# Kernel optimization log

Measured on AMD Instinct MI355X. Metric: run time of the kernel, lower is better.

## Reference

```python
import jax, jax.numpy as jnp
import numpy as np

N_NODES = 100000
N_EDGES = 1600000
N_GRAPHS = 2000
IN_DIM, HID, OUT_DIM, N_CLS = 6, 256, 128, 60
EPS = 1e-5


def setup_inputs() -> dict:
    key = jax.random.key(0)
    ks = jax.random.split(key, 16)
    def lin(k, i, o):
        s = 1.0 / np.sqrt(i)
        k1, k2 = jax.random.split(k)
        return (jax.random.uniform(k1, (i, o), jnp.float32, -s, s),
                jax.random.uniform(k2, (o,), jnp.float32, -s, s))
    W_emb, b_emb = lin(ks[0], IN_DIM, HID)
    Wc1, bc1 = lin(ks[1], HID, HID)
    W2, b2 = lin(ks[2], HID, HID)
    Wc2, bc2 = lin(ks[3], HID, HID)
    W3, b3 = lin(ks[4], HID, OUT_DIM)
    Wcls, bcls = lin(ks[5], OUT_DIM, N_CLS)
    return {
        'node_features': jax.random.normal(ks[6], (N_NODES, IN_DIM), jnp.float32),
        'src': jax.random.randint(ks[7], (N_EDGES,), 0, N_NODES, jnp.int32),
        'dst': jax.random.randint(ks[8], (N_EDGES,), 0, N_NODES, jnp.int32),
        'graph_ids': jnp.sort(jax.random.randint(ks[9], (N_NODES,), 0, N_GRAPHS, jnp.int32)),
        'W_emb': W_emb, 'b_emb': b_emb,
        'Wc1': Wc1, 'bc1': bc1,
        'g1': jnp.ones((HID,), jnp.float32), 'be1': jnp.zeros((HID,), jnp.float32),
        'W2': W2, 'b2': b2,
        'Wc2': Wc2, 'bc2': bc2,
        'g2': jnp.ones((HID,), jnp.float32), 'be2': jnp.zeros((HID,), jnp.float32),
        'W3': W3, 'b3': b3,
        'Wcls': Wcls, 'bcls': bcls,
    }


def _graph_conv(x, W, b, src, dst, dout_isqrt, din_isqrt):
    # DGL GraphConv, norm='both': msg = x_src * dout^-1/2, sum to dst, * din^-1/2, then W, b
    m = x[src] * dout_isqrt[src][:, None]            # [E, H]
    agg = jax.ops.segment_sum(m, dst, num_segments=N_NODES)
    agg = agg * din_isqrt[:, None]
    return agg @ W + b


def _bn(h, g, b):
    # BatchNorm1d, training mode: batch stats over node dim, biased variance
    mu = jnp.mean(h, axis=0)
    var = jnp.mean(jnp.square(h - mu), axis=0)
    return (h - mu) * jax.lax.rsqrt(var + EPS) * g + b


def reference(node_features, src, dst, graph_ids, W_emb, b_emb, Wc1, bc1, g1, be1,
              W2, b2, Wc2, bc2, g2, be2, W3, b3, Wcls, bcls):
    ones_e = jnp.ones((N_EDGES,), jnp.float32)
    dout = jax.ops.segment_sum(ones_e, src, num_segments=N_NODES)
    din = jax.ops.segment_sum(ones_e, dst, num_segments=N_NODES)
    dout_isqrt = jnp.where(dout > 0, jax.lax.rsqrt(jnp.maximum(dout, 1.0)), 0.0)
    din_isqrt = jnp.where(din > 0, jax.lax.rsqrt(jnp.maximum(din, 1.0)), 0.0)

    x = node_features @ W_emb + b_emb                              # [N, H]
    h = x + _graph_conv(x, Wc1, bc1, src, dst, dout_isqrt, din_isqrt)
    h = jax.nn.relu(_bn(h, g1, be1))
    h = h @ W2 + b2
    h = x + _graph_conv(h, Wc2, bc2, src, dst, dout_isqrt, din_isqrt)
    h = jax.nn.relu(_bn(h, g2, be2))
    h = h @ W3 + b3                                                # [N, OUT_DIM]

    # dgl.mean_nodes: per-graph mean of h
    sums = jax.ops.segment_sum(h, graph_ids, num_segments=N_GRAPHS)
    cnts = jax.ops.segment_sum(jnp.ones((N_NODES,), jnp.float32), graph_ids, num_segments=N_GRAPHS)
    y = sums / jnp.maximum(cnts, 1.0)[:, None]                     # [G, OUT_DIM]
    label = y @ Wcls + bcls                                        # [G, N_CLS]
    return h, label
```

## Files before the change

### kernel.cpp

```cpp
#include <hip/hip_runtime.h>

#define NNODES 100000
#define MPAD   100032
#define NEDGES 1600000
#define NGRAPHS 2000
#define HID 256
#define OUTD 128
#define NCLS 60
#define BN_EPS 1e-5f
#define NROWBLK 1563
#define NSCANBLK 98
#define REDBLK 32

typedef __attribute__((ext_vector_type(8))) short bf16x8;
typedef __attribute__((ext_vector_type(4))) float f32x4;

__device__ __forceinline__ float b2f(unsigned short b) {
    unsigned int u = ((unsigned int)b) << 16;
    return __builtin_bit_cast(float, u);
}
__device__ __forceinline__ unsigned short f2b(float f) {
    unsigned int u = __builtin_bit_cast(unsigned int, f);
    u = (u + 0x7FFFu + ((u >> 16) & 1u)) >> 16;
    return (unsigned short)u;
}

__global__ void k_zero_int(int* __restrict__ p, int n) {
    int i = blockIdx.x * blockDim.x + threadIdx.x;
    if (i < n) p[i] = 0;
}

__global__ void k_deg2(const int* __restrict__ src, const int* __restrict__ dst,
                       int* __restrict__ dout, int* __restrict__ din,
                       int* __restrict__ lpos) {
    int e = blockIdx.x * blockDim.x + threadIdx.x;
    if (e < NEDGES) {
        atomicAdd(&dout[src[e]], 1);
        lpos[e] = atomicAdd(&din[dst[e]], 1);
    }
}

__global__ void k_isqrt(const int* __restrict__ dout, const int* __restrict__ din,
                        float* __restrict__ dos, float* __restrict__ dis) {
    int i = blockIdx.x * blockDim.x + threadIdx.x;
    if (i < NNODES) {
        int a = dout[i], b = din[i];
        dos[i] = a > 0 ? 1.0f / sqrtf((float)a) : 0.0f;
        dis[i] = b > 0 ? 1.0f / sqrtf((float)b) : 0.0f;
    }
}

__global__ void k_blk_sum(const int* __restrict__ deg, int* __restrict__ bsum) {
    __shared__ int red[256];
    int blk = blockIdx.x, tid = threadIdx.x;
    int base = blk * 1024;
    int s = 0;
#pragma unroll
    for (int j = 0; j < 4; ++j) {
        int i = base + tid + j * 256;
        if (i < NNODES) s += deg[i];
    }
    red[tid] = s;
    __syncthreads();
    for (int off = 128; off > 0; off >>= 1) {
        if (tid < off) red[tid] += red[tid + off];
        __syncthreads();
    }
    if (tid == 0) bsum[blk] = red[0];
}

__global__ void k_scan_bsum(int* __restrict__ bsum) {
    if (threadIdx.x == 0) {
        int acc = 0;
        for (int i = 0; i < NSCANBLK; ++i) { int v = bsum[i]; bsum[i] = acc; acc += v; }
    }
}

__global__ void k_scan_local(const int* __restrict__ deg, const int* __restrict__ bsum,
                             int* __restrict__ row_ptr) {
    __shared__ int buf[1024];
    int blk = blockIdx.x, tid = threadIdx.x;
    int i = blk * 1024 + tid;
    int v = (i < NNODES) ? deg[i] : 0;
    buf[tid] = v;
    __syncthreads();
    for (int off = 1; off < 1024; off <<= 1) {
        int t = (tid >= off) ? buf[tid - off] : 0;
        __syncthreads();
        buf[tid] += t;
        __syncthreads();
    }
    int inc = buf[tid] + bsum[blk];
    if (i < NNODES) row_ptr[i + 1] = inc;
    if (i == 0) row_ptr[0] = 0;
}

__global__ void k_place(const int* __restrict__ src, const int* __restrict__ dst,
                        const int* __restrict__ lpos, const int* __restrict__ row_ptr,
                        const float* __restrict__ dos, int2* __restrict__ csr_ew) {
    int e = blockIdx.x * blockDim.x + threadIdx.x;
    if (e < NEDGES) {
        int s = src[e];
        csr_ew[row_ptr[dst[e]] + lpos[e]] = make_int2(s, __float_as_int(dos[s]));
    }
}

__global__ void k_wconv(const float* __restrict__ W, unsigned short* __restrict__ Wt,
                        int K, int N) {
    int idx = blockIdx.x * 256 + threadIdx.x;
    if (idx >= N * K) return;
    int n = idx / K, k = idx - n * K;
    Wt[idx] = f2b(W[(size_t)k * N + n]);
}

__global__ void k_small_mm(const float* __restrict__ Wemb, const float* __restrict__ bemb,
                           const float* __restrict__ Wc1, float* __restrict__ M1,
                           float* __restrict__ v1) {
    int c = threadIdx.x;
    int bi = blockIdx.x;
    float acc = 0.f;
    if (bi < 6) {
        for (int k = 0; k < HID; ++k) acc = fmaf(Wemb[bi * HID + k], Wc1[k * HID + c], acc);
        M1[bi * HID + c] = acc;
    } else {
        for (int k = 0; k < HID; ++k) acc = fmaf(bemb[k], Wc1[k * HID + c], acc);
        v1[c] = acc;
    }
}

__global__ void k_agg6(const int* __restrict__ row_ptr, const int2* __restrict__ csr_ew,
                       const float* __restrict__ nf,
                       float* __restrict__ t6, float* __restrict__ u1) {
    int n = blockIdx.x * blockDim.x + threadIdx.x;
    if (n >= NNODES) return;
    float a0 = 0, a1 = 0, a2 = 0, a3 = 0, a4 = 0, a5 = 0, au = 0;
    int s = row_ptr[n], e = row_ptr[n + 1];
    int i = s;
    for (; i + 2 <= e; i += 2) {
        int2 g0 = csr_ew[i], g1 = csr_ew[i + 1];
        float w0 = __int_as_float(g0.y), w1 = __int_as_float(g1.y);
        const float* p0 = nf + (size_t)g0.x * 6;
        const float* p1 = nf + (size_t)g1.x * 6;
        a0 = fmaf(w0, p0[0], a0); a1 = fmaf(w0, p0[1], a1); a2 = fmaf(w0, p0[2], a2);
        a3 = fmaf(w0, p0[3], a3); a4 = fmaf(w0, p0[4], a4); a5 = fmaf(w0, p0[5], a5);
        au += w0;
        a0 = fmaf(w1, p1[0], a0); a1 = fmaf(w1, p1[1], a1); a2 = fmaf(w1, p1[2], a2);
        a3 = fmaf(w1, p1[3], a3); a4 = fmaf(w1, p1[4], a4); a5 = fmaf(w1, p1[5], a5);
        au += w1;
    }
    for (; i < e; ++i) {
        int2 g0 = csr_ew[i];
        float w = __int_as_float(g0.y);
        const float* p = nf + (size_t)g0.x * 6;
        a0 = fmaf(w, p[0], a0); a1 = fmaf(w, p[1], a1); a2 = fmaf(w, p[2], a2);
        a3 = fmaf(w, p[3], a3); a4 = fmaf(w, p[4], a4); a5 = fmaf(w, p[5], a5);
        au += w;
    }
    float* t = t6 + (size_t)n * 6;
    t[0] = a0; t[1] = a1; t[2] = a2; t[3] = a3; t[4] = a4; t[5] = a5;
    u1[n] = au;
}

__global__ __launch_bounds__(256) void k_layer1(
    const float* __restrict__ nf, const float* __restrict__ Wemb, const float* __restrict__ bemb,
    const float* __restrict__ M1, const float* __restrict__ v1, const float* __restrict__ bc1,
    const float* __restrict__ t6, const float* __restrict__ u1, const float* __restrict__ dis,
    unsigned short* __restrict__ H, float* __restrict__ psum, float* __restrict__ psq) {
    __shared__ float s_nf[64][6];
    __shared__ float s_t6[64][6];
    __shared__ float s_u[64];
    __shared__ float s_r[64];
    int blk = blockIdx.x;
    int n0 = blk * 64;
    int tid = threadIdx.x;
    for (int t = tid; t < 384; t += 256) {
        int nl = t / 6, i = t % 6;
        int n = n0 + nl;
        s_nf[nl][i] = (n < NNODES) ? nf[(size_t)n * 6 + i] : 0.f;
        s_t6[nl][i] = (n < NNODES) ? t6[(size_t)n * 6 + i] : 0.f;
    }
    if (tid < 64) {
        int n = n0 + tid;
        s_u[tid] = (n < NNODES) ? u1[n] : 0.f;
        s_r[tid] = (n < NNODES) ? dis[n] : 0.f;
    }
    int c = tid;
    float wc[6], mc[6];
#pragma unroll
    for (int i = 0; i < 6; ++i) { wc[i] = Wemb[i * HID + c]; mc[i] = M1[i * HID + c]; }
    float v1c = v1[c];
    float bsum = bemb[c] + bc1[c];
    __syncthreads();
    float ps = 0.f, pq = 0.f;
    int nmax = min(64, NNODES - n0);
    for (int nl = 0; nl < nmax; ++nl) {
        float nfd = 0.f, td = 0.f;
#pragma unroll
        for (int i = 0; i < 6; ++i) {
            nfd = fmaf(s_nf[nl][i], wc[i], nfd);
            td = fmaf(s_t6[nl][i], mc[i], td);
        }
        float val = nfd + s_r[nl] * (td + s_u[nl] * v1c) + bsum;
        H[(size_t)(n0 + nl) * HID + c] = f2b(val);
        ps += val;
        pq = fmaf(val, val, pq);
    }
    for (int nl = nmax; nl < 64; ++nl) H[(size_t)(n0 + nl) * HID + c] = 0;
    psum[blk * HID + c] = ps;
    psq[blk * HID + c] = pq;
}

__global__ void k_bn_part(const float* __restrict__ psum, const float* __restrict__ psq,
                          double* __restrict__ tmp) {
    int c = threadIdx.x;
    int s = blockIdx.x;
    double a = 0.0, b = 0.0;
    for (int bb = s; bb < NROWBLK; bb += REDBLK) {
        a += psum[bb * HID + c];
        b += psq[bb * HID + c];
    }
    tmp[s * HID + c] = a;
    tmp[(REDBLK + s) * HID + c] = b;
}

__global__ void k_bn_final(const double* __restrict__ tmp, const float* __restrict__ g,
                           const float* __restrict__ be, float* __restrict__ scale,
                           float* __restrict__ shift) {
    int c = threadIdx.x;
    double s = 0.0, q = 0.0;
    for (int i = 0; i < REDBLK; ++i) { s += tmp[i * HID + c]; q += tmp[(REDBLK + i) * HID + c]; }
    double mu = s / (double)NNODES;
    double var = q / (double)NNODES - mu * mu;
    if (var < 0.0) var = 0.0;
    double inv = 1.0 / sqrt(var + (double)BN_EPS);
    float sc = (float)((double)g[c] * inv);
    scale[c] = sc;
    shift[c] = be[c] - (float)mu * sc;
}

template <int NC, bool ATRANS, bool XEPI, bool PART, bool OUTF32>
__global__ __launch_bounds__(256, 2) void k_mgemm(
    const unsigned short* __restrict__ A, const unsigned short* __restrict__ Bt,
    const float* __restrict__ bias,
    const float* __restrict__ scale, const float* __restrict__ shift,
    const float* __restrict__ nf, const float* __restrict__ Wemb, const float* __restrict__ bemb,
    unsigned short* __restrict__ Cb, float* __restrict__ Cf,
    float* __restrict__ psum, float* __restrict__ psq) {
    __shared__ unsigned short As[64 * 256];
    __shared__ unsigned short Bs[64 * 256];
    __shared__ float sSc[HID];
    __shared__ float sSh[HID];
    __shared__ float sNf[64][6];
    __shared__ float sXW[6][HID];
    __shared__ float redS[2][64];
    __shared__ float redQ[2][64];

    int tid = threadIdx.x;
    int rb = blockIdx.x;
    int row0 = rb * 64;

    if (ATRANS) { sSc[tid] = scale[tid]; sSh[tid] = shift[tid]; }
    if (XEPI) {
        for (int t = tid; t < 6 * NC; t += 256) {
            int i = t / NC, cl = t % NC;
            sXW[i][cl] = Wemb[i * HID + cl];
        }
        if (tid < 64) {
            int n = row0 + tid;
#pragma unroll
            for (int i = 0; i < 6; ++i) sNf[tid][i] = (n < NNODES) ? nf[(size_t)n * 6 + i] : 0.f;
        }
    }
    if (ATRANS) __syncthreads();

#pragma unroll
    for (int i = 0; i < 8; ++i) {
        int g = i * 256 + tid;
        int row = g >> 5, kc = g & 31;
        uint4 v = *(const uint4*)(A + (size_t)(row0 + row) * 256 + kc * 8);
        if (ATRANS) {
            unsigned int w[4] = {v.x, v.y, v.z, v.w};
#pragma unroll
            for (int q = 0; q < 4; ++q) {
                int k0 = kc * 8 + q * 2;
                float f0 = b2f((unsigned short)(w[q] & 0xffffu));
                float f1 = b2f((unsigned short)(w[q] >> 16));
                f0 = fmaxf(fmaf(f0, sSc[k0], sSh[k0]), 0.f);
                f1 = fmaxf(fmaf(f1, sSc[k0 + 1], sSh[k0 + 1]), 0.f);
                w[q] = (unsigned int)f2b(f0) | ((unsigned int)f2b(f1) << 16);
            }
            v.x = w[0]; v.y = w[1]; v.z = w[2]; v.w = w[3];
        }
        int pkc = kc ^ (row & 7);
        *(uint4*)(&As[row * 256 + pkc * 8]) = v;
    }

    int w = tid >> 6, lane = tid & 63;
    int wm = w >> 1, wn = w & 1;
    int lrow = lane & 15, lk = lane >> 4;

    for (int cb = 0; cb < NC / 64; ++cb) {
        int c0 = cb * 64;
        if (cb) __syncthreads();
#pragma unroll
        for (int i = 0; i < 8; ++i) {
            int g = i * 256 + tid;
            int row = g >> 5, kc = g & 31;
            uint4 v = *(const uint4*)(Bt + (size_t)(c0 + row) * 256 + kc * 8);
            int pkc = kc ^ (row & 7);
            *(uint4*)(&Bs[row * 256 + pkc * 8]) = v;
        }
        __syncthreads();

        f32x4 acc[2][2] = {};
#pragma unroll
        for (int ks = 0; ks < 8; ++ks) {
            bf16x8 af[2], bfr[2];
#pragma unroll
            for (int fm = 0; fm < 2; ++fm) {
                int r = wm * 32 + fm * 16 + lrow;
                int kc = ks * 4 + lk;
                af[fm] = *(const bf16x8*)(&As[r * 256 + (kc ^ (r & 7)) * 8]);
            }
#pragma unroll
            for (int fn = 0; fn < 2; ++fn) {
                int r = wn * 32 + fn * 16 + lrow;
                int kc = ks * 4 + lk;
                bfr[fn] = *(const bf16x8*)(&Bs[r * 256 + (kc ^ (r & 7)) * 8]);
            }
#pragma unroll
            for (int fm = 0; fm < 2; ++fm)
#pragma unroll
                for (int fn = 0; fn < 2; ++fn)
                    acc[fm][fn] = __builtin_amdgcn_mfma_f32_16x16x32_bf16(af[fm], bfr[fn], acc[fm][fn], 0, 0, 0);
        }

        float pS[2] = {0.f, 0.f}, pQ[2] = {0.f, 0.f};
#pragma unroll
        for (int fn = 0; fn < 2; ++fn) {
            int cl = wn * 32 + fn * 16 + lrow;
            int gc = c0 + cl;
            float bv = bias[gc];
            if (XEPI) bv += bemb[gc];
#pragma unroll
            for (int fm = 0; fm < 2; ++fm) {
#pragma unroll
                for (int r = 0; r < 4; ++r) {
                    int rl = wm * 32 + fm * 16 + lk * 4 + r;
                    int gr = row0 + rl;
                    float val = acc[fm][fn][r] + bv;
                    if (XEPI) {
#pragma unroll
                        for (int l = 0; l < 6; ++l) val = fmaf(sNf[rl][l], sXW[l][gc], val);
                    }
                    if (gr < NNODES) {
                        if (OUTF32) Cf[(size_t)gr * NC + gc] = val;
                        else        Cb[(size_t)gr * NC + gc] = f2b(val);
                        if (PART) { pS[fn] += val; pQ[fn] = fmaf(val, val, pQ[fn]); }
                    }
                }
            }
        }
        if (PART) {
#pragma unroll
            for (int fn = 0; fn < 2; ++fn) {
                float s = pS[fn], q = pQ[fn];
                s += __shfl_xor(s, 16); s += __shfl_xor(s, 32);
                q += __shfl_xor(q, 16); q += __shfl_xor(q, 32);
                if (lk == 0) {
                    int cl = wn * 32 + fn * 16 + lrow;
                    redS[wm][cl] = s;
                    redQ[wm][cl] = q;
                }
            }
            __syncthreads();
            if (tid < 64) {
                psum[(size_t)rb * HID + c0 + tid] = redS[0][tid] + redS[1][tid];
                psq [(size_t)rb * HID + c0 + tid] = redQ[0][tid] + redQ[1][tid];
            }
        }
    }
}

#define ACC8(vv, ww) { \
    a[0] = fmaf(ww, b2f((unsigned short)(vv.x & 0xffffu)), a[0]); \
    a[1] = fmaf(ww, b2f((unsigned short)(vv.x >> 16)),     a[1]); \
    a[2] = fmaf(ww, b2f((unsigned short)(vv.y & 0xffffu)), a[2]); \
    a[3] = fmaf(ww, b2f((unsigned short)(vv.y >> 16)),     a[3]); \
    a[4] = fmaf(ww, b2f((unsigned short)(vv.z & 0xffffu)), a[4]); \
    a[5] = fmaf(ww, b2f((unsigned short)(vv.z >> 16)),     a[5]); \
    a[6] = fmaf(ww, b2f((unsigned short)(vv.w & 0xffffu)), a[6]); \
    a[7] = fmaf(ww, b2f((unsigned short)(vv.w >> 16)),     a[7]); }

__global__ __launch_bounds__(256) void k_agg(const int* __restrict__ row_ptr,
                                             const int2* __restrict__ csr_ew,
                                             const unsigned short* __restrict__ X,
                                             const float* __restrict__ dis,
                                             unsigned short* __restrict__ out) {
    int wid = threadIdx.x >> 6, lane = threadIdx.x & 63;
    int half = lane >> 5, l32 = lane & 31;
    int n = blockIdx.x * 4 + wid;
    if (n >= NNODES) return;
    int s = row_ptr[n], e = row_ptr[n + 1];
    float a[8] = {0.f, 0.f, 0.f, 0.f, 0.f, 0.f, 0.f, 0.f};
    int i = s;
    for (; i + 8 <= e; i += 8) {
        int2 e0 = csr_ew[i + half];
        int2 e1 = csr_ew[i + 2 + half];
        int2 e2 = csr_ew[i + 4 + half];
        int2 e3 = csr_ew[i + 6 + half];
        uint4 v0 = ((const uint4*)(X + (size_t)e0.x * HID))[l32];
        uint4 v1 = ((const uint4*)(X + (size_t)e1.x * HID))[l32];
        uint4 v2 = ((const uint4*)(X + (size_t)e2.x * HID))[l32];
        uint4 v3 = ((const uint4*)(X + (size_t)e3.x * HID))[l32];
        float w0 = __int_as_float(e0.y), w1 = __int_as_float(e1.y);
        float w2 = __int_as_float(e2.y), w3 = __int_as_float(e3.y);
        ACC8(v0, w0) ACC8(v1, w1) ACC8(v2, w2) ACC8(v3, w3)
    }
    for (; i + 2 <= e; i += 2) {
        int2 e0 = csr_ew[i + half];
        uint4 v0 = ((const uint4*)(X + (size_t)e0.x * HID))[l32];
        float w0 = __int_as_float(e0.y);
        ACC8(v0, w0)
    }
    if (i < e && half == 0) {
        int2 e0 = csr_ew[i];
        uint4 v0 = ((const uint4*)(X + (size_t)e0.x * HID))[l32];
        float w0 = __int_as_float(e0.y);
        ACC8(v0, w0)
    }
#pragma unroll
    for (int j = 0; j < 8; ++j) a[j] += __shfl_xor(a[j], 32);
    if (half == 0) {
        float r = dis[n];
        uint4 o;
        o.x = (unsigned)f2b(a[0] * r) | ((unsigned)f2b(a[1] * r) << 16);
        o.y = (unsigned)f2b(a[2] * r) | ((unsigned)f2b(a[3] * r) << 16);
        o.z = (unsigned)f2b(a[4] * r) | ((unsigned)f2b(a[5] * r) << 16);
        o.w = (unsigned)f2b(a[6] * r) | ((unsigned)f2b(a[7] * r) << 16);
        ((uint4*)(out + (size_t)n * HID))[l32] = o;
    }
}

__global__ __launch_bounds__(128) void k_mean_label(const float* __restrict__ Hout,
                                                    const int* __restrict__ gids,
                                                    const float* __restrict__ Wcls,
                                                    const float* __restrict__ bcls,
                                                    float* __restrict__ lab) {
    int g = blockIdx.x;
    int c = threadIdx.x;
    int lo = 0, hi = NNODES;
    while (lo < hi) { int mid = (lo + hi) >> 1; if (gids[mid] < g) lo = mid + 1; else hi = mid; }
    int s = lo;
    hi = NNODES;
    while (lo < hi) { int mid = (lo + hi) >> 1; if (gids[mid] < g + 1) lo = mid + 1; else hi = mid; }
    int e = lo;
    float acc = 0.f;
    for (int n = s; n < e; ++n) acc += Hout[(size_t)n * OUTD + c];
    int cnt = e - s;
    float y = acc / (float)max(cnt, 1);
    __shared__ float ys[OUTD];
    ys[c] = y;
    __syncthreads();
    if (c < NCLS) {
        float a = bcls[c];
        for (int k = 0; k < OUTD; ++k) a = fmaf(ys[k], Wcls[k * NCLS + c], a);
        lab[(size_t)g * NCLS + c] = a;
    }
}

extern "C" void kernel_launch(void* const* d_in, const int* in_sizes, int n_in,
                              void* d_out, int out_size, void* d_ws, size_t ws_size,
                              hipStream_t stream) {
    const float* nf   = (const float*)d_in[0];
    const int*   src  = (const int*)d_in[1];
    const int*   dst  = (const int*)d_in[2];
    const int*   gids = (const int*)d_in[3];
    const float* Wemb = (const float*)d_in[4];
    const float* bemb = (const float*)d_in[5];
    const float* Wc1  = (const float*)d_in[6];
    const float* bc1  = (const float*)d_in[7];
    const float* g1   = (const float*)d_in[8];
    const float* be1  = (const float*)d_in[9];
    const float* W2   = (const float*)d_in[10];
    const float* b2   = (const float*)d_in[11];
    const float* Wc2  = (const float*)d_in[12];
    const float* bc2  = (const float*)d_in[13];
    const float* g2   = (const float*)d_in[14];
    const float* be2  = (const float*)d_in[15];
    const float* W3   = (const float*)d_in[16];
    const float* b3   = (const float*)d_in[17];
    const float* Wcls = (const float*)d_in[18];
    const float* bcls = (const float*)d_in[19];

    float* out_h   = (float*)d_out;
    float* out_lab = out_h + (size_t)NNODES * OUTD;

    float* ws = (float*)d_ws;
    size_t off = 0;
    auto take = [&](size_t n) { float* p = ws + off; off += (n + 63) & ~(size_t)63; return p; };
    unsigned short* actA = (unsigned short*)take((size_t)MPAD * HID / 2);
    unsigned short* actB = (unsigned short*)take((size_t)MPAD * HID / 2);
    unsigned short* Wt2  = (unsigned short*)take(HID * HID / 2);
    unsigned short* Wtc2 = (unsigned short*)take(HID * HID / 2);
    unsigned short* Wt3  = (unsigned short*)take(OUTD * HID / 2);
    int*   deg_out = (int*)take(NNODES);
    int*   deg_in  = (int*)take(NNODES);
    float* dout_is = take(NNODES);
    float* din_is  = take(NNODES);
    int*   row_ptr = (int*)take(NNODES + 1);
    int*   lpos    = (int*)take(NEDGES);
    int2*  csr_ew  = (int2*)take((size_t)NEDGES * 2);
    float* t6      = take((size_t)NNODES * 6);
    float* u1      = take(NNODES);
    float* M1      = take(6 * HID);
    float* v1      = take(HID);
    float* psum    = take((size_t)NROWBLK * HID);
    float* psq     = take((size_t)NROWBLK * HID);
    float* scale1  = take(HID);
    float* shift1  = take(HID);
    float* scale2  = take(HID);
    float* shift2  = take(HID);
    int*   bsum    = (int*)take(128);
    double* bn_tmp = (double*)take(2 * 2 * REDBLK * HID);

    k_zero_int<<<(2 * 100032 + 255) / 256, 256, 0, stream>>>(deg_out, 2 * 100032);
    k_deg2<<<(NEDGES + 255) / 256, 256, 0, stream>>>(src, dst, deg_out, deg_in, lpos);
    k_isqrt<<<(NNODES + 255) / 256, 256, 0, stream>>>(deg_out, deg_in, dout_is, din_is);
    k_blk_sum<<<NSCANBLK, 256, 0, stream>>>(deg_in, bsum);
    k_scan_bsum<<<1, 64, 0, stream>>>(bsum);
    k_scan_local<<<NSCANBLK, 1024, 0, stream>>>(deg_in, bsum, row_ptr);
    k_place<<<(NEDGES + 255) / 256, 256, 0, stream>>>(src, dst, lpos, row_ptr, dout_is, csr_ew);
    k_wconv<<<(HID * HID + 255) / 256, 256, 0, stream>>>(W2, Wt2, HID, HID);
    k_wconv<<<(HID * HID + 255) / 256, 256, 0, stream>>>(Wc2, Wtc2, HID, HID);
    k_wconv<<<(HID * OUTD + 255) / 256, 256, 0, stream>>>(W3, Wt3, HID, OUTD);
    k_small_mm<<<7, 256, 0, stream>>>(Wemb, bemb, Wc1, M1, v1);
    k_agg6<<<(NNODES + 255) / 256, 256, 0, stream>>>(row_ptr, csr_ew, nf, t6, u1);
    k_layer1<<<NROWBLK, 256, 0, stream>>>(nf, Wemb, bemb, M1, v1, bc1, t6, u1, din_is,
                                          actA, psum, psq);
    k_bn_part<<<REDBLK, 256, 0, stream>>>(psum, psq, bn_tmp);
    k_bn_final<<<1, 256, 0, stream>>>(bn_tmp, g1, be1, scale1, shift1);
    k_mgemm<HID, true, false, false, false><<<NROWBLK, 256, 0, stream>>>(
        actA, Wt2, b2, scale1, shift1, nullptr, nullptr, nullptr, actB, nullptr, nullptr, nullptr);
    k_agg<<<NNODES / 4, 256, 0, stream>>>(row_ptr, csr_ew, actB, din_is, actA);
    k_mgemm<HID, false, true, true, false><<<NROWBLK, 256, 0, stream>>>(
        actA, Wtc2, bc2, nullptr, nullptr, nf, Wemb, bemb, actB, nullptr, psum, psq);
    k_bn_part<<<REDBLK, 256, 0, stream>>>(psum, psq, bn_tmp);
    k_bn_final<<<1, 256, 0, stream>>>(bn_tmp, g2, be2, scale2, shift2);
    k_mgemm<OUTD, true, false, false, true><<<NROWBLK, 256, 0, stream>>>(
        actB, Wt3, b3, scale2, shift2, nullptr, nullptr, nullptr, nullptr, out_h, nullptr, nullptr);
    k_mean_label<<<NGRAPHS, OUTD, 0, stream>>>(out_h, gids, Wcls, bcls, out_lab);
}
```

Before: 724.0 us.

## Pre-scale sources by out-degree norm to shrink CSR to bare indices

Moves the per-edge out-degree normalization into the producers: the layer-1 GEMM epilogue scales its rows by dout^-1/2, and the raw features are pre-scaled into a padded 8-float array that also carries the weight for the u-term. The CSR then stores only source indices (4 bytes per edge instead of 8), and both aggregation kernels use plain adds with vectorized float4 loads. It also fuses the isqrt kernel into the block-sum kernel and merges three weight-conversion launches into one. The cost is an extra nf7 pass and an additional bf16 rounding of the pre-scaled activations.

```diff
diff --git a/kernel.cpp b/kernel.cpp
--- a/kernel.cpp
+++ b/kernel.cpp
@@ -40,17 +40,9 @@
     }
 }
 
-__global__ void k_isqrt(const int* __restrict__ dout, const int* __restrict__ din,
-                        float* __restrict__ dos, float* __restrict__ dis) {
-    int i = blockIdx.x * blockDim.x + threadIdx.x;
-    if (i < NNODES) {
-        int a = dout[i], b = din[i];
-        dos[i] = a > 0 ? 1.0f / sqrtf((float)a) : 0.0f;
-        dis[i] = b > 0 ? 1.0f / sqrtf((float)b) : 0.0f;
-    }
-}
-
-__global__ void k_blk_sum(const int* __restrict__ deg, int* __restrict__ bsum) {
+__global__ void k_blk_sum(const int* __restrict__ din, const int* __restrict__ dout,
+                          int* __restrict__ bsum, float* __restrict__ dos,
+                          float* __restrict__ dis) {
     __shared__ int red[256];
     int blk = blockIdx.x, tid = threadIdx.x;
     int base = blk * 1024;
@@ -58,7 +50,13 @@
 #pragma unroll
     for (int j = 0; j < 4; ++j) {
         int i = base + tid + j * 256;
-        if (i < NNODES) s += deg[i];
+        if (i < NNODES) {
+            int b = din[i];
+            int a = dout[i];
+            s += b;
+            dos[i] = a > 0 ? 1.0f / sqrtf((float)a) : 0.0f;
+            dis[i] = b > 0 ? 1.0f / sqrtf((float)b) : 0.0f;
+        }
     }
     red[tid] = s;
     __syncthreads();
@@ -97,20 +95,39 @@
 
 __global__ void k_place(const int* __restrict__ src, const int* __restrict__ dst,
                         const int* __restrict__ lpos, const int* __restrict__ row_ptr,
-                        const float* __restrict__ dos, int2* __restrict__ csr_ew) {
+                        int* __restrict__ csr_e) {
     int e = blockIdx.x * blockDim.x + threadIdx.x;
-    if (e < NEDGES) {
-        int s = src[e];
-        csr_ew[row_ptr[dst[e]] + lpos[e]] = make_int2(s, __float_as_int(dos[s]));
-    }
-}
-
-__global__ void k_wconv(const float* __restrict__ W, unsigned short* __restrict__ Wt,
-                        int K, int N) {
+    if (e < NEDGES) csr_e[row_ptr[dst[e]] + lpos[e]] = src[e];
+}
+
+__global__ void k_nf7(const float* __restrict__ nf, const float* __restrict__ dos,
+                      float* __restrict__ nf7) {
+    int n = blockIdx.x * blockDim.x + threadIdx.x;
+    if (n >= NNODES) return;
+    float w = dos[n];
+    const float* p = nf + (size_t)n * 6;
+    float4 lo = {p[0] * w, p[1] * w, p[2] * w, p[3] * w};
+    float4 hi = {p[4] * w, p[5] * w, w, 0.f};
+    float4* o = (float4*)(nf7 + (size_t)n * 8);
+    o[0] = lo; o[1] = hi;
+}
+
+__global__ void k_wconv3(const float* __restrict__ W2, const float* __restrict__ Wc2,
+                         const float* __restrict__ W3, unsigned short* __restrict__ Wt2,
+                         unsigned short* __restrict__ Wtc2, unsigned short* __restrict__ Wt3) {
     int idx = blockIdx.x * 256 + threadIdx.x;
-    if (idx >= N * K) return;
-    int n = idx / K, k = idx - n * K;
-    Wt[idx] = f2b(W[(size_t)k * N + n]);
+    if (idx < 65536) {
+        int n = idx >> 8, k = idx & 255;
+        Wt2[idx] = f2b(W2[k * 256 + n]);
+    } else if (idx < 131072) {
+        int j = idx - 65536;
+        int n = j >> 8, k = j & 255;
+        Wtc2[j] = f2b(Wc2[k * 256 + n]);
+    } else if (idx < 163840) {
+        int j = idx - 131072;
+        int n = j >> 8, k = j & 255;
+        Wt3[j] = f2b(W3[k * 128 + n]);
+    }
 }
 
 __global__ void k_small_mm(const float* __restrict__ Wemb, const float* __restrict__ bemb,
@@ -128,47 +145,37 @@
     }
 }
 
-__global__ void k_agg6(const int* __restrict__ row_ptr, const int2* __restrict__ csr_ew,
-                       const float* __restrict__ nf,
-                       float* __restrict__ t6, float* __restrict__ u1) {
+__global__ void k_agg6(const int* __restrict__ row_ptr, const int* __restrict__ csr_e,
+                       const float* __restrict__ nf7, float* __restrict__ t7) {
     int n = blockIdx.x * blockDim.x + threadIdx.x;
     if (n >= NNODES) return;
-    float a0 = 0, a1 = 0, a2 = 0, a3 = 0, a4 = 0, a5 = 0, au = 0;
+    float a0 = 0, a1 = 0, a2 = 0, a3 = 0, a4 = 0, a5 = 0, a6 = 0;
     int s = row_ptr[n], e = row_ptr[n + 1];
     int i = s;
     for (; i + 2 <= e; i += 2) {
-        int2 g0 = csr_ew[i], g1 = csr_ew[i + 1];
-        float w0 = __int_as_float(g0.y), w1 = __int_as_float(g1.y);
-        const float* p0 = nf + (size_t)g0.x * 6;
-        const float* p1 = nf + (size_t)g1.x * 6;
-        a0 = fmaf(w0, p0[0], a0); a1 = fmaf(w0, p0[1], a1); a2 = fmaf(w0, p0[2], a2);
-        a3 = fmaf(w0, p0[3], a3); a4 = fmaf(w0, p0[4], a4); a5 = fmaf(w0, p0[5], a5);
-        au += w0;
-        a0 = fmaf(w1, p1[0], a0); a1 = fmaf(w1, p1[1], a1); a2 = fmaf(w1, p1[2], a2);
-        a3 = fmaf(w1, p1[3], a3); a4 = fmaf(w1, p1[4], a4); a5 = fmaf(w1, p1[5], a5);
-        au += w1;
-    }
-    for (; i < e; ++i) {
-        int2 g0 = csr_ew[i];
-        float w = __int_as_float(g0.y);
-        const float* p = nf + (size_t)g0.x * 6;
-        a0 = fmaf(w, p[0], a0); a1 = fmaf(w, p[1], a1); a2 = fmaf(w, p[2], a2);
-        a3 = fmaf(w, p[3], a3); a4 = fmaf(w, p[4], a4); a5 = fmaf(w, p[5], a5);
-        au += w;
-    }
-    float* t = t6 + (size_t)n * 6;
-    t[0] = a0; t[1] = a1; t[2] = a2; t[3] = a3; t[4] = a4; t[5] = a5;
-    u1[n] = au;
+        const float4* p0 = (const float4*)(nf7 + (size_t)csr_e[i] * 8);
+        const float4* p1 = (const float4*)(nf7 + (size_t)csr_e[i + 1] * 8);
+        float4 l0 = p0[0], h0 = p0[1], l1 = p1[0], h1 = p1[1];
+        a0 += l0.x; a1 += l0.y; a2 += l0.z; a3 += l0.w; a4 += h0.x; a5 += h0.y; a6 += h0.z;
+        a0 += l1.x; a1 += l1.y; a2 += l1.z; a3 += l1.w; a4 += h1.x; a5 += h1.y; a6 += h1.z;
+    }
+    if (i < e) {
+        const float4* p0 = (const float4*)(nf7 + (size_t)csr_e[i] * 8);
+        float4 l0 = p0[0], h0 = p0[1];
+        a0 += l0.x; a1 += l0.y; a2 += l0.z; a3 += l0.w; a4 += h0.x; a5 += h0.y; a6 += h0.z;
+    }
+    float4* o = (float4*)(t7 + (size_t)n * 8);
+    o[0] = make_float4(a0, a1, a2, a3);
+    o[1] = make_float4(a4, a5, a6, 0.f);
 }
 
 __global__ __launch_bounds__(256) void k_layer1(
     const float* __restrict__ nf, const float* __restrict__ Wemb, const float* __restrict__ bemb,
     const float* __restrict__ M1, const float* __restrict__ v1, const float* __restrict__ bc1,
-    const float* __restrict__ t6, const float* __restrict__ u1, const float* __restrict__ dis,
+    const float* __restrict__ t7, const float* __restrict__ dis,
     unsigned short* __restrict__ H, float* __restrict__ psum, float* __restrict__ psq) {
     __shared__ float s_nf[64][6];
-    __shared__ float s_t6[64][6];
-    __shared__ float s_u[64];
+    __shared__ float s_t7[64][8];
     __shared__ float s_r[64];
     int blk = blockIdx.x;
     int n0 = blk * 64;
@@ -177,11 +184,11 @@
         int nl = t / 6, i = t % 6;
         int n = n0 + nl;
         s_nf[nl][i] = (n < NNODES) ? nf[(size_t)n * 6 + i] : 0.f;
-        s_t6[nl][i] = (n < NNODES) ? t6[(size_t)n * 6 + i] : 0.f;
-    }
+    }
+    if (tid < 128)
+        ((float4*)s_t7)[tid] = ((const float4*)(t7 + (size_t)n0 * 8))[tid];
     if (tid < 64) {
         int n = n0 + tid;
-        s_u[tid] = (n < NNODES) ? u1[n] : 0.f;
         s_r[tid] = (n < NNODES) ? dis[n] : 0.f;
     }
     int c = tid;
@@ -198,9 +205,9 @@
 #pragma unroll
         for (int i = 0; i < 6; ++i) {
             nfd = fmaf(s_nf[nl][i], wc[i], nfd);
-            td = fmaf(s_t6[nl][i], mc[i], td);
-        }
-        float val = nfd + s_r[nl] * (td + s_u[nl] * v1c) + bsum;
+            td = fmaf(s_t7[nl][i], mc[i], td);
+        }
+        float val = nfd + s_r[nl] * (td + s_t7[nl][6] * v1c) + bsum;
         H[(size_t)(n0 + nl) * HID + c] = f2b(val);
         ps += val;
         pq = fmaf(val, val, pq);
@@ -238,12 +245,13 @@
     shift[c] = be[c] - (float)mu * sc;
 }
 
-template <int NC, bool ATRANS, bool XEPI, bool PART, bool OUTF32>
+template <int NC, bool ATRANS, bool XEPI, bool PART, bool OUTF32, bool RS>
 __global__ __launch_bounds__(256, 2) void k_mgemm(
     const unsigned short* __restrict__ A, const unsigned short* __restrict__ Bt,
     const float* __restrict__ bias,
     const float* __restrict__ scale, const float* __restrict__ shift,
     const float* __restrict__ nf, const float* __restrict__ Wemb, const float* __restrict__ bemb,
+    const float* __restrict__ rs,
     unsigned short* __restrict__ Cb, float* __restrict__ Cf,
     float* __restrict__ psum, float* __restrict__ psq) {
     __shared__ unsigned short As[64 * 256];
@@ -252,6 +260,7 @@
     __shared__ float sSh[HID];
     __shared__ float sNf[64][6];
     __shared__ float sXW[6][HID];
+    __shared__ float sRs[64];
     __shared__ float redS[2][64];
     __shared__ float redQ[2][64];
 
@@ -260,6 +269,10 @@
     int row0 = rb * 64;
 
     if (ATRANS) { sSc[tid] = scale[tid]; sSh[tid] = shift[tid]; }
+    if (RS && tid < 64) {
+        int n = row0 + tid;
+        sRs[tid] = (n < NNODES) ? rs[n] : 0.f;
+    }
     if (XEPI) {
         for (int t = tid; t < 6 * NC; t += 256) {
             int i = t / NC, cl = t % NC;
@@ -353,6 +366,7 @@
 #pragma unroll
                         for (int l = 0; l < 6; ++l) val = fmaf(sNf[rl][l], sXW[l][gc], val);
                     }
+                    if (RS) val *= sRs[rl];
                     if (gr < NNODES) {
                         if (OUTF32) Cf[(size_t)gr * NC + gc] = val;
                         else        Cb[(size_t)gr * NC + gc] = f2b(val);
@@ -382,18 +396,18 @@
     }
 }
 
-#define ACC8(vv, ww) { \
-    a[0] = fmaf(ww, b2f((unsigned short)(vv.x & 0xffffu)), a[0]); \
-    a[1] = fmaf(ww, b2f((unsigned short)(vv.x >> 16)),     a[1]); \
-    a[2] = fmaf(ww, b2f((unsigned short)(vv.y & 0xffffu)), a[2]); \
-    a[3] = fmaf(ww, b2f((unsigned short)(vv.y >> 16)),     a[3]); \
-    a[4] = fmaf(ww, b2f((unsigned short)(vv.z & 0xffffu)), a[4]); \
-    a[5] = fmaf(ww, b2f((unsigned short)(vv.z >> 16)),     a[5]); \
-    a[6] = fmaf(ww, b2f((unsigned short)(vv.w & 0xffffu)), a[6]); \
-    a[7] = fmaf(ww, b2f((unsigned short)(vv.w >> 16)),     a[7]); }
+#define ADD8(vv) { \
+    a[0] += b2f((unsigned short)(vv.x & 0xffffu)); \
+    a[1] += b2f((unsigned short)(vv.x >> 16)); \
+    a[2] += b2f((unsigned short)(vv.y & 0xffffu)); \
+    a[3] += b2f((unsigned short)(vv.y >> 16)); \
+    a[4] += b2f((unsigned short)(vv.z & 0xffffu)); \
+    a[5] += b2f((unsigned short)(vv.z >> 16)); \
+    a[6] += b2f((unsigned short)(vv.w & 0xffffu)); \
+    a[7] += b2f((unsigned short)(vv.w >> 16)); }
 
 __global__ __launch_bounds__(256) void k_agg(const int* __restrict__ row_ptr,
-                                             const int2* __restrict__ csr_ew,
+                                             const int* __restrict__ csr_e,
                                              const unsigned short* __restrict__ X,
                                              const float* __restrict__ dis,
                                              unsigned short* __restrict__ out) {
@@ -405,29 +419,25 @@
     float a[8] = {0.f, 0.f, 0.f, 0.f, 0.f, 0.f, 0.f, 0.f};
     int i = s;
     for (; i + 8 <= e; i += 8) {
-        int2 e0 = csr_ew[i + half];
-        int2 e1 = csr_ew[i + 2 + half];
-        int2 e2 = csr_ew[i + 4 + half];
-        int2 e3 = csr_ew[i + 6 + half];
-        uint4 v0 = ((const uint4*)(X + (size_t)e0.x * HID))[l32];
-        uint4 v1 = ((const uint4*)(X + (size_t)e1.x * HID))[l32];
-        uint4 v2 = ((const uint4*)(X + (size_t)e2.x * HID))[l32];
-        uint4 v3 = ((const uint4*)(X + (size_t)e3.x * HID))[l32];
-        float w0 = __int_as_float(e0.y), w1 = __int_as_float(e1.y);
-        float w2 = __int_as_float(e2.y), w3 = __int_as_float(e3.y);
-        ACC8(v0, w0) ACC8(v1, w1) ACC8(v2, w2) ACC8(v3, w3)
+        int s0 = csr_e[i + half];
+        int s1 = csr_e[i + 2 + half];
+        int s2 = csr_e[i + 4 + half];
+        int s3 = csr_e[i + 6 + half];
+        uint4 v0 = ((const uint4*)(X + (size_t)s0 * HID))[l32];
+        uint4 v1 = ((const uint4*)(X + (size_t)s1 * HID))[l32];
+        uint4 v2 = ((const uint4*)(X + (size_t)s2 * HID))[l32];
+        uint4 v3 = ((const uint4*)(X + (size_t)s3 * HID))[l32];
+        ADD8(v0) ADD8(v1) ADD8(v2) ADD8(v3)
     }
     for (; i + 2 <= e; i += 2) {
-        int2 e0 = csr_ew[i + half];
-        uint4 v0 = ((const uint4*)(X + (size_t)e0.x * HID))[l32];
-        float w0 = __int_as_float(e0.y);
-        ACC8(v0, w0)
+        int s0 = csr_e[i + half];
+        uint4 v0 = ((const uint4*)(X + (size_t)s0 * HID))[l32];
+        ADD8(v0)
     }
     if (i < e && half == 0) {
-        int2 e0 = csr_ew[i];
-        uint4 v0 = ((const uint4*)(X + (size_t)e0.x * HID))[l32];
-        float w0 = __int_as_float(e0.y);
-        ACC8(v0, w0)
+        int s0 = csr_e[i];
+        uint4 v0 = ((const uint4*)(X + (size_t)s0 * HID))[l32];
+        ADD8(v0)
     }
 #pragma unroll
     for (int j = 0; j < 8; ++j) a[j] += __shfl_xor(a[j], 32);
@@ -510,9 +520,9 @@
     float* din_is  = take(NNODES);
     int*   row_ptr = (int*)take(NNODES + 1);
     int*   lpos    = (int*)take(NEDGES);
-    int2*  csr_ew  = (int2*)take((size_t)NEDGES * 2);
-    float* t6      = take((size_t)NNODES * 6);
-    float* u1      = take(NNODES);
+    int*   csr_e   = (int*)take(NEDGES);
+    float* nf7     = take((size_t)NNODES * 8);
+    float* t7      = take((size_t)MPAD * 8);
     float* M1      = take(6 * HID);
     float* v1      = take(HID);
     float* psum    = take((size_t)NROWBLK * HID);
@@ -526,28 +536,29 @@
 
     k_zero_int<<<(2 * 100032 + 255) / 256, 256, 0, stream>>>(deg_out, 2 * 100032);
     k_deg2<<<(NEDGES + 255) / 256, 256, 0, stream>>>(src, dst, deg_out, deg_in, lpos);
-    k_isqrt<<<(NNODES + 255) / 256, 256, 0, stream>>>(deg_out, deg_in, dout_is, din_is);
-    k_blk_sum<<<NSCANBLK, 256, 0, stream>>>(deg_in, bsum);
+    k_blk_sum<<<NSCANBLK, 256, 0, stream>>>(deg_in, deg_out, bsum, dout_is, din_is);
     k_scan_bsum<<<1, 64, 0, stream>>>(bsum);
     k_scan_local<<<NSCANBLK, 1024, 0, stream>>>(deg_in, bsum, row_ptr);
-    k_place<<<(NEDGES + 255) / 256, 256, 0, stream>>>(src, dst, lpos, row_ptr, dout_is, csr_ew);
-    k_wconv<<<(HID * HID + 255) / 256, 256, 0, stream>>>(W2, Wt2, HID, HID);
-    k_wconv<<<(HID * HID + 255) / 256, 256, 0, stream>>>(Wc2, Wtc2, HID, HID);
-    k_wconv<<<(HID * OUTD + 255) / 256, 256, 0, stream>>>(W3, Wt3, HID, OUTD);
+    k_place<<<(NEDGES + 255) / 256, 256, 0, stream>>>(src, dst, lpos, row_ptr, csr_e);
+    k_nf7<<<(NNODES + 255) / 256, 256, 0, stream>>>(nf, dout_is, nf7);
+    k_wconv3<<<640, 256, 0, stream>>>(W2, Wc2, W3, Wt2, Wtc2, Wt3);
     k_small_mm<<<7, 256, 0, stream>>>(Wemb, bemb, Wc1, M1, v1);
-    k_agg6<<<(NNODES + 255) / 256, 256, 0, stream>>>(row_ptr, csr_ew, nf, t6, u1);
-    k_layer1<<<NROWBLK, 256, 0, stream>>>(nf, Wemb, bemb, M1, v1, bc1, t6, u1, din_is,
+    k_agg6<<<(NNODES + 255) / 256, 256, 0, stream>>>(row_ptr, csr_e, nf7, t7);
+    k_layer1<<<NROWBLK, 256, 0, stream>>>(nf, Wemb, bemb, M1, v1, bc1, t7, din_is,
                                           actA, psum, psq);
     k_bn_part<<<REDBLK, 256, 0, stream>>>(psum, psq, bn_tmp);
     k_bn_final<<<1, 256, 0, stream>>>(bn_tmp, g1, be1, scale1, shift1);
-    k_mgemm<HID, true, false, false, false><<<NROWBLK, 256, 0, stream>>>(
-        actA, Wt2, b2, scale1, shift1, nullptr, nullptr, nullptr, actB, nullptr, nullptr, nullptr);
-    k_agg<<<NNODES / 4, 256, 0, stream>>>(row_ptr, csr_ew, actB, din_is, actA);
-    k_mgemm<HID, false, true, true, false><<<NROWBLK, 256, 0, stream>>>(
-        actA, Wtc2, bc2, nullptr, nullptr, nf, Wemb, bemb, actB, nullptr, psum, psq);
+    k_mgemm<HID, true, false, false, false, true><<<NROWBLK, 256, 0, stream>>>(
+        actA, Wt2, b2, scale1, shift1, nullptr, nullptr, nullptr, dout_is,
+        actB, nullptr, nullptr, nullptr);
+    k_agg<<<NNODES / 4, 256, 0, stream>>>(row_ptr, csr_e, actB, din_is, actA);
+    k_mgemm<HID, false, true, true, false, false><<<NROWBLK, 256, 0, stream>>>(
+        actA, Wtc2, bc2, nullptr, nullptr, nf, Wemb, bemb, nullptr,
+        actB, nullptr, psum, psq);
     k_bn_part<<<REDBLK, 256, 0, stream>>>(psum, psq, bn_tmp);
     k_bn_final<<<1, 256, 0, stream>>>(bn_tmp, g2, be2, scale2, shift2);
-    k_mgemm<OUTD, true, false, false, true><<<NROWBLK, 256, 0, stream>>>(
-        actB, Wt3, b3, scale2, shift2, nullptr, nullptr, nullptr, nullptr, out_h, nullptr, nullptr);
+    k_mgemm<OUTD, true, false, false, true, false><<<NROWBLK, 256, 0, stream>>>(
+        actB, Wt3, b3, scale2, shift2, nullptr, nullptr, nullptr, nullptr,
+        nullptr, out_h, nullptr, nullptr);
     k_mean_label<<<NGRAPHS, OUTD, 0, stream>>>(out_h, gids, Wcls, bcls, out_lab);
 }
```

Result: no change. 720.8 us (-0.4%).
